# Kernel tuning notes

Measured on AMD Instinct MI355X. Metric: run time of the kernel, lower is better.

Reference implementation:

```python
import jax, jax.numpy as jnp
import numpy as np

N_NODES = 50000
N_RAND_EDGES = 800000
K_HEADS = 4
D = 64
EPS = 1e-8


def setup_inputs() -> dict:
    key = jax.random.key(0)
    k1, k2, k3, k4, k5, k6 = jax.random.split(key, 6)
    x = jax.random.normal(k1, (N_NODES, D), dtype=jnp.float32)
    # edge_index without self loops (module removes then re-adds them), then append self loops
    dst = jax.random.randint(k2, (N_RAND_EDGES,), 0, N_NODES)
    off = jax.random.randint(k3, (N_RAND_EDGES,), 1, N_NODES)
    src = (dst + off) % N_NODES  # guaranteed src != dst
    loops = jnp.arange(N_NODES)
    adj = jnp.stack([jnp.concatenate([dst, loops]), jnp.concatenate([src, loops])]).astype(jnp.int64)
    e = jax.random.uniform(k4, (N_NODES, K_HEADS), dtype=jnp.float32)
    stdv = 1.0 / np.sqrt(D)
    weights = jax.random.uniform(k5, (K_HEADS, D, D), minval=-stdv, maxval=stdv, dtype=jnp.float32)
    # xavier_uniform(gain=1.414) on [K, 2D, 1]
    bound = 1.414 * np.sqrt(6.0 / (2 * D + 1))
    a = jax.random.uniform(k6, (K_HEADS, 2 * D, 1), minval=-bound, maxval=bound, dtype=jnp.float32)
    return {"x": x, "adj": adj, "e": e, "weights": weights, "a": a}


def reference(x, adj, e, weights, a):
    N = x.shape[0]
    O = weights.shape[2]
    dst, src = adj[0], adj[1]  # aggregation destination = adj[0], source = adj[1]
    # per-head projection: h[k] = x @ weights[k]  -> [K, N, O]
    h = jnp.einsum('nd,kdo->kno', x, weights)
    # split attention vector: edge_h @ a == <h[dst], a[:O]> + <h[src], a[O:]>
    a_dst = a[:, :O, 0]   # [K, O]
    a_src = a[:, O:, 0]   # [K, O]
    alpha_dst = jnp.einsum('kno,ko->kn', h, a_dst)  # [K, N]
    alpha_src = jnp.einsum('kno,ko->kn', h, a_src)  # [K, N]
    logits = jax.nn.leaky_relu(alpha_dst[:, dst] + alpha_src[:, src], 0.01)  # [K, E]
    # global (per-head) max subtraction, as in the original
    edge_e = jnp.exp(logits - jnp.max(logits, axis=1, keepdims=True))  # [K, E]
    seg = lambda v: jax.ops.segment_sum(v, dst, num_segments=N)
    denom = jax.vmap(seg)(edge_e) + EPS                                 # [K, N]
    num = jax.vmap(seg)(edge_e[:, :, None] * h[:, src])                 # [K, N, O]
    outputs = num / denom[:, :, None]                                   # [K, N, O]
    out = jnp.einsum('nk,kno->no', e, outputs)                          # mixture over K
    return out + x  # residual
```

## Files before the change

### kernel.cpp

```cpp
#include <hip/hip_runtime.h>
#include <hip/hip_bf16.h>

#define KH 4
#define DIM 64
#define EPSV 1e-8f
#define CSTRIDE 16

typedef __attribute__((ext_vector_type(8))) short bf16x8;
typedef __attribute__((ext_vector_type(4))) float f32x4;
typedef __attribute__((ext_vector_type(2))) float f32x2;

__device__ __forceinline__ float lrelu(float s) { return s > 0.0f ? s : 0.01f * s; }
__device__ __forceinline__ float blo(unsigned u) { return __uint_as_float(u << 16); }
__device__ __forceinline__ float bhi(unsigned u) { return __uint_as_float(u & 0xFFFF0000u); }
__device__ __forceinline__ unsigned short f2b(float f) {
    unsigned u = __float_as_uint(f);
    u += 0x7FFFu + ((u >> 16) & 1u);
    return (unsigned short)(u >> 16);
}

__device__ __forceinline__ unsigned char f2e4m3(float f) {
    unsigned u = __float_as_uint(f);
    unsigned sgn = (u >> 31) << 7;
    float af = fabsf(f);
    if (af >= 0.015625f) {
        unsigned mag = u & 0x7FFFFFFFu;
        unsigned biased = mag - (120u << 23);
        unsigned em = biased >> 20;
        unsigned rem = biased & 0xFFFFFu;
        em += (rem > 0x80000u) ? 1u : ((rem == 0x80000u) ? (em & 1u) : 0u);
        if (em > 126u) em = 126u;
        return (unsigned char)(sgn | em);
    } else {
        int m = (int)rintf(af * 512.0f);
        if (m >= 8) return (unsigned char)(sgn | 8u);
        return (unsigned char)(sgn | (unsigned)m);
    }
}

__device__ __forceinline__ void e4m3x4_to_f32(unsigned v, float& h0, float& h1,
                                              float& h2, float& h3) {
#if __has_builtin(__builtin_amdgcn_cvt_pk_f32_fp8)
    f32x2 lo = __builtin_amdgcn_cvt_pk_f32_fp8(v, false);
    f32x2 hi = __builtin_amdgcn_cvt_pk_f32_fp8(v, true);
    h0 = lo.x; h1 = lo.y; h2 = hi.x; h3 = hi.y;
#else
    auto dec = [](unsigned b) -> float {
        unsigned s = b >> 7, em = b & 0x7Fu;
        float r;
        if (em >= 8u) r = __uint_as_float((em << 20) + (120u << 23));
        else r = (float)em * 0.001953125f;
        return s ? -r : r;
    };
    h0 = dec(v & 0xFF); h1 = dec((v >> 8) & 0xFF);
    h2 = dec((v >> 16) & 0xFF); h3 = dec(v >> 24);
#endif
}

__global__ void __launch_bounds__(256, 4)
k_hidden(const float* __restrict__ x,
         const float* __restrict__ W,
         const float* __restrict__ a,
         unsigned* __restrict__ h8,
         float* __restrict__ adst,
         float* __restrict__ asrc,
         int* __restrict__ cnt, int N) {
    int t = threadIdx.x;
    int gid = blockIdx.x * 256 + t;
    if (gid < N * CSTRIDE) cnt[gid] = 0;
    int k = t >> 6;
    int l = t & 63;
    int s = l & 15;
    int q = l >> 4;
    int n0 = blockIdx.x * 16;

    const float* Wk = W + k * DIM * DIM;
    bf16x8 Bf[4][2];
#pragma unroll
    for (int tile = 0; tile < 4; ++tile)
#pragma unroll
        for (int c = 0; c < 2; ++c) {
            const float* wp = Wk + (size_t)(32 * c + 8 * q) * DIM + 16 * tile + s;
#pragma unroll
            for (int j = 0; j < 8; ++j)
                Bf[tile][c][j] = (short)f2b(wp[(size_t)j * DIM]);
        }
    float ad[4], as_[4];
#pragma unroll
    for (int tile = 0; tile < 4; ++tile) {
        ad[tile]  = a[k * 2 * DIM + 16 * tile + s];
        as_[tile] = a[k * 2 * DIM + DIM + 16 * tile + s];
    }

    bf16x8 Af[2];
#pragma unroll
    for (int c = 0; c < 2; ++c) {
        const float* xp = x + (size_t)(n0 + s) * DIM + 32 * c + 8 * q;
#pragma unroll
        for (int j = 0; j < 8; ++j) Af[c][j] = (short)f2b(xp[j]);
    }

    f32x4 acc[4];
#pragma unroll
    for (int tile = 0; tile < 4; ++tile) {
        acc[tile] = (f32x4){0.f, 0.f, 0.f, 0.f};
#pragma unroll
        for (int c = 0; c < 2; ++c)
            acc[tile] = __builtin_amdgcn_mfma_f32_16x16x32_bf16(
                Af[c], Bf[tile][c], acc[tile], 0, 0, 0);
    }

#pragma unroll
    for (int r = 0; r < 4; ++r) {
        float vd = 0.f, vs = 0.f;
#pragma unroll
        for (int tile = 0; tile < 4; ++tile) {
            vd = fmaf(acc[tile][r], ad[tile], vd);
            vs = fmaf(acc[tile][r], as_[tile], vs);
        }
#pragma unroll
        for (int off = 1; off < 16; off <<= 1) {
            vd += __shfl_xor(vd, off);
            vs += __shfl_xor(vs, off);
        }
        if (s == 0) {
            int n = n0 + 4 * q + r;
            adst[n * KH + k] = vd;
            asrc[n * KH + k] = vs;
        }
    }

    __shared__ unsigned char hb[16 * DIM * KH];
#pragma unroll
    for (int tile = 0; tile < 4; ++tile)
#pragma unroll
        for (int r = 0; r < 4; ++r) {
            int n = 4 * q + r, o = 16 * tile + s;
            int word = n * DIM + (o ^ (q << 4));
            hb[word * KH + k] = f2e4m3(acc[tile][r]);
        }
    __syncthreads();
    const unsigned* hb4 = (const unsigned*)hb;
#pragma unroll
    for (int it = 0; it < 4; ++it) {
        int w = it * 256 + t;
        int wp = w ^ ((((unsigned)w >> 8) & 3u) << 4);
        h8[(size_t)n0 * DIM + w] = hb4[wp];
    }
}

__global__ void k_bin(const int* __restrict__ dst, const int* __restrict__ src,
                      const float4* __restrict__ adst4, const float4* __restrict__ asrc4,
                      int* __restrict__ cnt, uint4* __restrict__ slots,
                      int cap, int E) {
    int tid = blockIdx.x * blockDim.x + threadIdx.x;
    int e0 = tid * 2;
    if (e0 >= E) return;
    int2 d = ((const int2*)dst)[tid];
    int2 s = ((const int2*)src)[tid];
    int sl0 = atomicAdd(&cnt[d.x * CSTRIDE], 1);
    int sl1 = atomicAdd(&cnt[d.y * CSTRIDE], 1);
    float4 ad0 = adst4[d.x], as0 = asrc4[s.x];
    float4 ad1 = adst4[d.y], as1 = asrc4[s.y];
#define EMIT(sl, dn, sn, ad, as)                                              \
    if (sl < cap) {                                                           \
        uint4 sv;                                                             \
        sv.x = (unsigned)sn;                                                  \
        sv.y = (unsigned)f2b(__expf(lrelu(ad.x + as.x))) |                    \
               ((unsigned)f2b(__expf(lrelu(ad.y + as.y))) << 16);             \
        sv.z = (unsigned)f2b(__expf(lrelu(ad.z + as.z))) |                    \
               ((unsigned)f2b(__expf(lrelu(ad.w + as.w))) << 16);             \
        sv.w = 0u;                                                            \
        slots[(size_t)dn * cap + sl] = sv;                                    \
    }
    EMIT(sl0, d.x, s.x, ad0, as0)
    EMIT(sl1, d.y, s.y, ad1, as1)
#undef EMIT
}

__global__ void __launch_bounds__(256, 8)
k_aggr(const int* __restrict__ cnt, const uint4* __restrict__ slots,
       const unsigned* __restrict__ h8,
       const float* __restrict__ efeat, const float* __restrict__ x,
       float* __restrict__ out, int cap, int N) {
    int n = __builtin_amdgcn_readfirstlane(blockIdx.x * 4 + (threadIdx.x >> 6));
    if (n >= N) return;
    int o = threadIdx.x & 63;
    int deg = cnt[n * CSTRIDE]; if (deg > cap) deg = cap;
    const uint4* bs = slots + (size_t)n * cap;
    float v0 = 0.f, v1 = 0.f, v2 = 0.f, v3 = 0.f;
    float d0 = 0.f, d1 = 0.f, d2 = 0.f, d3 = 0.f;
#define ACC(sv, hv)                                                           \
    {                                                                         \
        float h0, h1, h2, h3;                                                 \
        e4m3x4_to_f32(hv, h0, h1, h2, h3);                                    \
        float w;                                                              \
        w = blo(sv.y); v0 = fmaf(w, h0, v0); d0 += w;                         \
        w = bhi(sv.y); v1 = fmaf(w, h1, v1); d1 += w;                         \
        w = blo(sv.z); v2 = fmaf(w, h2, v2); d2 += w;                         \
        w = bhi(sv.z); v3 = fmaf(w, h3, v3); d3 += w;                         \
    }
    int i = 0;
    for (; i + 4 <= deg; i += 4) {
        uint4 s0 = bs[i + 0], s1 = bs[i + 1], s2 = bs[i + 2], s3 = bs[i + 3];
        unsigned a0 = h8[(size_t)s0.x * DIM + o];
        unsigned a1 = h8[(size_t)s1.x * DIM + o];
        unsigned a2 = h8[(size_t)s2.x * DIM + o];
        unsigned a3 = h8[(size_t)s3.x * DIM + o];
        ACC(s0, a0) ACC(s1, a1) ACC(s2, a2) ACC(s3, a3)
    }
    for (; i < deg; ++i) {
        uint4 sv = bs[i];
        unsigned hv = h8[(size_t)sv.x * DIM + o];
        ACC(sv, hv)
    }
#undef ACC
    float4 ef = ((const float4*)efeat)[n];
    float c0 = ef.x / (d0 + EPSV), c1 = ef.y / (d1 + EPSV);
    float c2 = ef.z / (d2 + EPSV), c3 = ef.w / (d3 + EPSV);
    size_t oi = (size_t)n * DIM + o;
    out[oi] = x[oi] + c0 * v0 + c1 * v1 + c2 * v2 + c3 * v3;
}

extern "C" void kernel_launch(void* const* d_in, const int* in_sizes, int n_in,
                              void* d_out, int out_size, void* d_ws, size_t ws_size,
                              hipStream_t stream) {
    const float* x = (const float*)d_in[0];
    const int* adj = (const int*)d_in[1];
    const float* efeat = (const float*)d_in[2];
    const float* W = (const float*)d_in[3];
    const float* a = (const float*)d_in[4];
    float* out = (float*)d_out;

    int N = in_sizes[0] / DIM;
    int E = in_sizes[1] / 2;
    const int* dst = adj;
    const int* src = adj + E;
    int nbhid = (N + 15) / 16;

    unsigned* h8 = (unsigned*)d_ws;
    float* adst = (float*)(h8 + (size_t)N * DIM);
    float* asrc = adst + (size_t)N * KH;
    int* cnt = (int*)(asrc + (size_t)N * KH);
    uint4* slots = (uint4*)(cnt + (size_t)N * CSTRIDE);
    size_t used = (size_t)((char*)slots - (char*)d_ws);
    int cap = (int)((ws_size - used) / ((size_t)N * 16));
    if (cap > 64) cap = 64;

    k_hidden<<<nbhid, 256, 0, stream>>>(x, W, a, h8, adst, asrc, cnt, N);

    int npair = E / 2;
    k_bin<<<(npair + 255) / 256, 256, 0, stream>>>(dst, src, (const float4*)adst,
                                                   (const float4*)asrc, cnt,
                                                   slots, cap, E);

    k_aggr<<<(N + 3) / 4, 256, 0, stream>>>(cnt, slots, h8, efeat, x, out, cap, N);
}
```

Measured before the change: 170.8 us.

## Move edge weight computation from binning into aggregation kernel, store only src indices

The binning kernel now writes only the 4-byte source index per edge slot instead of a 16-byte record holding precomputed bf16 attention weights. The aggregation kernel loads the per-node alpha_dst once and gathers alpha_src per edge to recompute exp(leaky_relu(.)) in fp32. This cuts slot write and read traffic roughly fourfold and removes the gathers from the atomic-heavy binning pass. In exchange it adds a float4 gather plus four exps per edge on every lane of the aggregation wavefront, where previously each lane only unpacked bf16 weights.

Measured after the change: 214.9 us. +25.8%, slower.

```diff
diff --git a/kernel.cpp b/kernel.cpp
--- a/kernel.cpp
+++ b/kernel.cpp
@@ -11,8 +11,6 @@
 typedef __attribute__((ext_vector_type(2))) float f32x2;
 
 __device__ __forceinline__ float lrelu(float s) { return s > 0.0f ? s : 0.01f * s; }
-__device__ __forceinline__ float blo(unsigned u) { return __uint_as_float(u << 16); }
-__device__ __forceinline__ float bhi(unsigned u) { return __uint_as_float(u & 0xFFFF0000u); }
 __device__ __forceinline__ unsigned short f2b(float f) {
     unsigned u = __float_as_uint(f);
     u += 0x7FFFu + ((u >> 16) & 1u);
@@ -150,69 +148,57 @@
 }
 
 __global__ void k_bin(const int* __restrict__ dst, const int* __restrict__ src,
-                      const float4* __restrict__ adst4, const float4* __restrict__ asrc4,
-                      int* __restrict__ cnt, uint4* __restrict__ slots,
+                      int* __restrict__ cnt, int* __restrict__ bsrc,
                       int cap, int E) {
     int tid = blockIdx.x * blockDim.x + threadIdx.x;
-    int e0 = tid * 2;
-    if (e0 >= E) return;
+    if (tid * 2 >= E) return;
     int2 d = ((const int2*)dst)[tid];
     int2 s = ((const int2*)src)[tid];
     int sl0 = atomicAdd(&cnt[d.x * CSTRIDE], 1);
     int sl1 = atomicAdd(&cnt[d.y * CSTRIDE], 1);
-    float4 ad0 = adst4[d.x], as0 = asrc4[s.x];
-    float4 ad1 = adst4[d.y], as1 = asrc4[s.y];
-#define EMIT(sl, dn, sn, ad, as)                                              \
-    if (sl < cap) {                                                           \
-        uint4 sv;                                                             \
-        sv.x = (unsigned)sn;                                                  \
-        sv.y = (unsigned)f2b(__expf(lrelu(ad.x + as.x))) |                    \
-               ((unsigned)f2b(__expf(lrelu(ad.y + as.y))) << 16);             \
-        sv.z = (unsigned)f2b(__expf(lrelu(ad.z + as.z))) |                    \
-               ((unsigned)f2b(__expf(lrelu(ad.w + as.w))) << 16);             \
-        sv.w = 0u;                                                            \
-        slots[(size_t)dn * cap + sl] = sv;                                    \
-    }
-    EMIT(sl0, d.x, s.x, ad0, as0)
-    EMIT(sl1, d.y, s.y, ad1, as1)
-#undef EMIT
+    if (sl0 < cap) bsrc[(size_t)d.x * cap + sl0] = s.x;
+    if (sl1 < cap) bsrc[(size_t)d.y * cap + sl1] = s.y;
 }
 
 __global__ void __launch_bounds__(256, 8)
-k_aggr(const int* __restrict__ cnt, const uint4* __restrict__ slots,
+k_aggr(const int* __restrict__ cnt, const int* __restrict__ bsrc,
        const unsigned* __restrict__ h8,
+       const float4* __restrict__ adst4, const float4* __restrict__ asrc4,
        const float* __restrict__ efeat, const float* __restrict__ x,
        float* __restrict__ out, int cap, int N) {
     int n = __builtin_amdgcn_readfirstlane(blockIdx.x * 4 + (threadIdx.x >> 6));
     if (n >= N) return;
     int o = threadIdx.x & 63;
     int deg = cnt[n * CSTRIDE]; if (deg > cap) deg = cap;
-    const uint4* bs = slots + (size_t)n * cap;
+    const int* bs = bsrc + (size_t)n * cap;
+    float4 adn = adst4[n];
     float v0 = 0.f, v1 = 0.f, v2 = 0.f, v3 = 0.f;
     float d0 = 0.f, d1 = 0.f, d2 = 0.f, d3 = 0.f;
-#define ACC(sv, hv)                                                           \
+#define ACC(qv, hv)                                                           \
     {                                                                         \
         float h0, h1, h2, h3;                                                 \
         e4m3x4_to_f32(hv, h0, h1, h2, h3);                                    \
         float w;                                                              \
-        w = blo(sv.y); v0 = fmaf(w, h0, v0); d0 += w;                         \
-        w = bhi(sv.y); v1 = fmaf(w, h1, v1); d1 += w;                         \
-        w = blo(sv.z); v2 = fmaf(w, h2, v2); d2 += w;                         \
-        w = bhi(sv.z); v3 = fmaf(w, h3, v3); d3 += w;                         \
+        w = __expf(lrelu(adn.x + qv.x)); v0 = fmaf(w, h0, v0); d0 += w;       \
+        w = __expf(lrelu(adn.y + qv.y)); v1 = fmaf(w, h1, v1); d1 += w;       \
+        w = __expf(lrelu(adn.z + qv.z)); v2 = fmaf(w, h2, v2); d2 += w;       \
+        w = __expf(lrelu(adn.w + qv.w)); v3 = fmaf(w, h3, v3); d3 += w;       \
     }
     int i = 0;
     for (; i + 4 <= deg; i += 4) {
-        uint4 s0 = bs[i + 0], s1 = bs[i + 1], s2 = bs[i + 2], s3 = bs[i + 3];
-        unsigned a0 = h8[(size_t)s0.x * DIM + o];
-        unsigned a1 = h8[(size_t)s1.x * DIM + o];
-        unsigned a2 = h8[(size_t)s2.x * DIM + o];
-        unsigned a3 = h8[(size_t)s3.x * DIM + o];
-        ACC(s0, a0) ACC(s1, a1) ACC(s2, a2) ACC(s3, a3)
+        int s0 = bs[i + 0], s1 = bs[i + 1], s2 = bs[i + 2], s3 = bs[i + 3];
+        float4 q0 = asrc4[s0], q1 = asrc4[s1], q2 = asrc4[s2], q3 = asrc4[s3];
+        unsigned a0 = h8[(size_t)s0 * DIM + o];
+        unsigned a1 = h8[(size_t)s1 * DIM + o];
+        unsigned a2 = h8[(size_t)s2 * DIM + o];
+        unsigned a3 = h8[(size_t)s3 * DIM + o];
+        ACC(q0, a0) ACC(q1, a1) ACC(q2, a2) ACC(q3, a3)
     }
     for (; i < deg; ++i) {
-        uint4 sv = bs[i];
-        unsigned hv = h8[(size_t)sv.x * DIM + o];
-        ACC(sv, hv)
+        int sn = bs[i];
+        float4 qv = asrc4[sn];
+        unsigned hv = h8[(size_t)sn * DIM + o];
+        ACC(qv, hv)
     }
 #undef ACC
     float4 ef = ((const float4*)efeat)[n];
@@ -242,17 +228,17 @@
     float* adst = (float*)(h8 + (size_t)N * DIM);
     float* asrc = adst + (size_t)N * KH;
     int* cnt = (int*)(asrc + (size_t)N * KH);
-    uint4* slots = (uint4*)(cnt + (size_t)N * CSTRIDE);
-    size_t used = (size_t)((char*)slots - (char*)d_ws);
-    int cap = (int)((ws_size - used) / ((size_t)N * 16));
+    int* bsrc = cnt + (size_t)N * CSTRIDE;
+    size_t used = (size_t)((char*)bsrc - (char*)d_ws);
+    int cap = (int)((ws_size - used) / ((size_t)N * 4));
     if (cap > 64) cap = 64;
 
     k_hidden<<<nbhid, 256, 0, stream>>>(x, W, a, h8, adst, asrc, cnt, N);
 
     int npair = E / 2;
-    k_bin<<<(npair + 255) / 256, 256, 0, stream>>>(dst, src, (const float4*)adst,
-                                                   (const float4*)asrc, cnt,
-                                                   slots, cap, E);
-
-    k_aggr<<<(N + 3) / 4, 256, 0, stream>>>(cnt, slots, h8, efeat, x, out, cap, N);
-}
+    k_bin<<<(npair + 255) / 256, 256, 0, stream>>>(dst, src, cnt, bsrc, cap, E);
+
+    k_aggr<<<(N + 3) / 4, 256, 0, stream>>>(cnt, bsrc, h8,
+                                            (const float4*)adst, (const float4*)asrc,
+                                            efeat, x, out, cap, N);
+}
```

## Partition edge binning by destination range across eight block groups

Applied to the files above, without the earlier changes.

The binning kernel now runs a fixed grid of 2048 blocks split into eight groups. Each group scans the whole edge list with a grid-stride loop and handles only edges whose destination falls in its slice of the node range. The aim is to keep the atomics, the alpha reads and the slot writes of each group inside a smaller, cache-friendly slice of nodes, likely matching the eight XCDs on MI355X. In exchange, every edge index is read eight times, and load balance now depends on how destinations are spread.

Measured after the change: 171.8 us. No clear change (+0.6%).

```diff
diff --git a/kernel.cpp b/kernel.cpp
--- a/kernel.cpp
+++ b/kernel.cpp
@@ -152,29 +152,36 @@
 __global__ void k_bin(const int* __restrict__ dst, const int* __restrict__ src,
                       const float4* __restrict__ adst4, const float4* __restrict__ asrc4,
                       int* __restrict__ cnt, uint4* __restrict__ slots,
-                      int cap, int E) {
-    int tid = blockIdx.x * blockDim.x + threadIdx.x;
-    int e0 = tid * 2;
-    if (e0 >= E) return;
-    int2 d = ((const int2*)dst)[tid];
-    int2 s = ((const int2*)src)[tid];
-    int sl0 = atomicAdd(&cnt[d.x * CSTRIDE], 1);
-    int sl1 = atomicAdd(&cnt[d.y * CSTRIDE], 1);
-    float4 ad0 = adst4[d.x], as0 = asrc4[s.x];
-    float4 ad1 = adst4[d.y], as1 = asrc4[s.y];
-#define EMIT(sl, dn, sn, ad, as)                                              \
-    if (sl < cap) {                                                           \
-        uint4 sv;                                                             \
-        sv.x = (unsigned)sn;                                                  \
-        sv.y = (unsigned)f2b(__expf(lrelu(ad.x + as.x))) |                    \
-               ((unsigned)f2b(__expf(lrelu(ad.y + as.y))) << 16);             \
-        sv.z = (unsigned)f2b(__expf(lrelu(ad.z + as.z))) |                    \
-               ((unsigned)f2b(__expf(lrelu(ad.w + as.w))) << 16);             \
-        sv.w = 0u;                                                            \
-        slots[(size_t)dn * cap + sl] = sv;                                    \
-    }
-    EMIT(sl0, d.x, s.x, ad0, as0)
-    EMIT(sl1, d.y, s.y, ad1, as1)
+                      int cap, int E, int N) {
+    int part = blockIdx.x & 7;
+    int sub = blockIdx.x >> 3;
+    int nsub = gridDim.x >> 3;
+    int lo = part * (N >> 3);
+    int hi = (part == 7) ? N : lo + (N >> 3);
+    int npair = E >> 1;
+    const int2* d2 = (const int2*)dst;
+    const int2* s2 = (const int2*)src;
+#define EMIT(dn, sn)                                                          \
+    {                                                                         \
+        int sl = atomicAdd(&cnt[(dn) * CSTRIDE], 1);                          \
+        if (sl < cap) {                                                       \
+            float4 ad = adst4[dn], as = asrc4[sn];                            \
+            uint4 sv;                                                         \
+            sv.x = (unsigned)(sn);                                            \
+            sv.y = (unsigned)f2b(__expf(lrelu(ad.x + as.x))) |                \
+                   ((unsigned)f2b(__expf(lrelu(ad.y + as.y))) << 16);         \
+            sv.z = (unsigned)f2b(__expf(lrelu(ad.z + as.z))) |                \
+                   ((unsigned)f2b(__expf(lrelu(ad.w + as.w))) << 16);         \
+            sv.w = 0u;                                                        \
+            slots[(size_t)(dn) * cap + sl] = sv;                              \
+        }                                                                     \
+    }
+    for (int p = sub * 256 + threadIdx.x; p < npair; p += nsub * 256) {
+        int2 d = d2[p];
+        int2 s = s2[p];
+        if (d.x >= lo && d.x < hi) EMIT(d.x, s.x)
+        if (d.y >= lo && d.y < hi) EMIT(d.y, s.y)
+    }
 #undef EMIT
 }
 
@@ -249,10 +256,8 @@
 
     k_hidden<<<nbhid, 256, 0, stream>>>(x, W, a, h8, adst, asrc, cnt, N);
 
-    int npair = E / 2;
-    k_bin<<<(npair + 255) / 256, 256, 0, stream>>>(dst, src, (const float4*)adst,
-                                                   (const float4*)asrc, cnt,
-                                                   slots, cap, E);
+    k_bin<<<2048, 256, 0, stream>>>(dst, src, (const float4*)adst,
+                                    (const float4*)asrc, cnt, slots, cap, E, N);
 
     k_aggr<<<(N + 3) / 4, 256, 0, stream>>>(cnt, slots, h8, efeat, x, out, cap, N);
 }
```
